# Performance work log

Measured on AMD Instinct MI355X. Metric: run time of the kernel, lower is better.

The kernel has to match this reference:

```python
import jax, jax.numpy as jnp
import numpy as np

N = 50000      # nodes
E = 800000     # edges (before self loops)
NF = 4         # node feature dim
EF = 4         # edge feature dim
EMB = 16       # joint embedding dim
HID = 64       # hidden dim
OUT = 128      # output dim
H = 4          # heads (layers 0,1); last layer has 1 head
NEG_SLOPE = 0.2


def setup_inputs() -> dict:
    key = jax.random.key(0)
    ks = jax.random.split(key, 20)
    in0 = NF + EMB  # 20

    def lin(k, o, i):
        return (jax.random.normal(k, (o, i), jnp.float32) * np.float32(1.0 / np.sqrt(i)))

    return {
        'x': jax.random.normal(ks[0], (N, NF), jnp.float32),
        'edge_index': jax.random.randint(ks[1], (2, E), 0, N, dtype=jnp.int32),
        'edge_attr': jax.random.normal(ks[2], (E, EF), jnp.float32),
        'joint_types': jax.random.randint(ks[3], (N,), 0, 17, dtype=jnp.int32),
        'emb_table': jax.random.normal(ks[4], (17, EMB), jnp.float32) * 0.1,
        'W0': lin(ks[5], H * HID, in0),
        'a_src0': jax.random.normal(ks[6], (H, HID), jnp.float32) * 0.1,
        'a_dst0': jax.random.normal(ks[7], (H, HID), jnp.float32) * 0.1,
        'We0': lin(ks[8], H, EF),
        'W1': lin(ks[9], H * HID, HID),
        'a_src1': jax.random.normal(ks[10], (H, HID), jnp.float32) * 0.1,
        'a_dst1': jax.random.normal(ks[11], (H, HID), jnp.float32) * 0.1,
        'We1': lin(ks[12], H, EF),
        'W2': lin(ks[13], 1 * OUT, HID),
        'a_src2': jax.random.normal(ks[14], (1, OUT), jnp.float32) * 0.1,
        'a_dst2': jax.random.normal(ks[15], (1, OUT), jnp.float32) * 0.1,
        'We2': lin(ks[16], 1, EF),
    }


def gat_layer(x, src, dst, eattr, W, a_src, a_dst, We, num_nodes):
    # x: [N, F_in]; W: [H*C, F_in]; a_src/a_dst: [H, C]; We: [H, EF]
    Hh, C = a_src.shape
    h = (x @ W.T).reshape(num_nodes, Hh, C)  # [N, H, C]
    # per-node attention scores, gathered per edge (same math as per-edge dot)
    s_i = jnp.einsum('nhc,hc->nh', h, a_src)  # applied to x_i = x[dst]
    s_j = jnp.einsum('nhc,hc->nh', h, a_dst)  # applied to x_j = x[src]
    alpha = s_i[dst] + s_j[src] + eattr @ We.T  # [Etot, H]
    alpha = jax.nn.leaky_relu(alpha, NEG_SLOPE)
    # faithful to torch.softmax(alpha, dim=0): GLOBAL softmax over all edges per head
    alpha = jax.nn.softmax(alpha, axis=0)
    msgs = h[src] * alpha[:, :, None]  # [Etot, H, C]
    out = jax.ops.segment_sum(msgs, dst, num_segments=num_nodes)  # aggr='add'
    return out.mean(axis=1)  # update(): mean over heads -> [N, C]


def reference(x, edge_index, edge_attr, joint_types, emb_table,
              W0, a_src0, a_dst0, We0,
              W1, a_src1, a_dst1, We1,
              W2, a_src2, a_dst2, We2):
    num_nodes = x.shape[0]
    # add self loops (edge_attr fill 0.0)
    loops = jnp.arange(num_nodes, dtype=edge_index.dtype)
    src = jnp.concatenate([edge_index[0], loops])
    dst = jnp.concatenate([edge_index[1], loops])
    eattr = jnp.concatenate([edge_attr, jnp.zeros((num_nodes, edge_attr.shape[1]), edge_attr.dtype)], axis=0)

    h = jnp.concatenate([x, emb_table[joint_types]], axis=-1)  # [N, 20]
    h = gat_layer(h, src, dst, eattr, W0, a_src0, a_dst0, We0, num_nodes)
    h = jax.nn.elu(h)  # dropout is identity in eval mode
    h = gat_layer(h, src, dst, eattr, W1, a_src1, a_dst1, We1, num_nodes)
    h = jax.nn.elu(h)
    h = gat_layer(h, src, dst, eattr, W2, a_src2, a_dst2, We2, num_nodes)
    return h  # [N, OUT]
```

## Files before the change

### kernel.cpp

```cpp
#include <hip/hip_runtime.h>
#include <math.h>

#define NN 50000
#define EE 800000
#define EEN (EE+NN)
#define STRIDE 64
#define NFEAT 4
#define EFEAT 4
#define EMBD 16
#define IN0 20
#define HIDD 64
#define OUTD 128

__device__ __forceinline__ unsigned short f2bf(float f){
  unsigned u = __float_as_uint(f);
  return (unsigned short)((u + 0x7FFFu + ((u>>16)&1u)) >> 16);
}
__device__ __forceinline__ float bfl(unsigned u){ return __uint_as_float(u<<16); }
__device__ __forceinline__ float bfh(unsigned u){ return __uint_as_float(u & 0xFFFF0000u); }

template<int V> struct ldt;
template<> struct ldt<4>{ using T = uint2; };
template<> struct ldt<2>{ using T = unsigned int; };

__global__ void k_init(int* fill){
  int i = blockIdx.x*blockDim.x + threadIdx.x;
  if (i < NN) fill[i]=0;
}

__global__ void k_scatter(const int* __restrict__ ei, int* fill,
                          int* __restrict__ col, int* __restrict__ epos){
  int idx = blockIdx.x*blockDim.x + threadIdx.x;
  if (idx < EE){
    int d = ei[EE+idx];
    int pos = atomicAdd(&fill[d],1);
    col[d*STRIDE + 1 + pos] = ei[idx];
    epos[idx] = d*STRIDE + 1 + pos;
  } else if (idx < EEN){
    int n = idx-EE;
    col[n*STRIDE] = n;
  }
}

template<int F_IN,int HH,int CC>
__device__ __forceinline__ void av_one(const float* W, const float* asrc,
                                       const float* adst, float* av, int tid){
  if (tid >= HH*F_IN) return;
  int h = tid / F_IN, f = tid % F_IN;
  float s1=0.f, s2=0.f;
  for (int c=0;c<CC;c++){
    float wv = W[(size_t)(h*CC+c)*F_IN+f];
    s1 += asrc[h*CC+c]*wv;
    s2 += adst[h*CC+c]*wv;
  }
  av[tid] = s1;
  av[HH*F_IN+tid] = s2;
}
__global__ void k_av3(const float* W0, const float* as0, const float* ad0, float* av0,
                      const float* W1, const float* as1, const float* ad1, float* av1,
                      const float* W2, const float* as2, const float* ad2, float* av2,
                      float* zred){
  int tid = threadIdx.x;
  if      (blockIdx.x==0){ av_one<IN0,4,64> (W0, as0, ad0, av0, tid); if (tid<24) zred[tid]=0.f; }
  else if (blockIdx.x==1) av_one<64,4,64>  (W1, as1, ad1, av1, tid);
  else                    av_one<64,1,128> (W2, as2, ad2, av2, tid);
}

template<int K,int NCOL,int HH,bool CONCAT>
__global__ __launch_bounds__(256)
void k_gemm(const float* __restrict__ xin, const int* __restrict__ jt,
            const float* __restrict__ emb, const float* __restrict__ W,
            const float* __restrict__ avp, unsigned short* __restrict__ hout,
            float* __restrict__ si, float* __restrict__ sj){
  constexpr int PITCH = 132;
  __shared__ float xT[K*PITCH];
  __shared__ float wT[K*PITCH];
  __shared__ float EMBL[CONCAT ? 17*EMBD : 1];
  int tid = threadIdx.x;
  int rbase = blockIdx.x*128, cbase = blockIdx.y*128;
  if (CONCAT){
    for (int i=tid; i<17*EMBD; i+=256) EMBL[i]=emb[i];
    __syncthreads();
    if (tid < 128){
      int row = tid;
      int gr = rbase+row; if (gr >= NN) gr = NN-1;
      float4 v = ((const float4*)xin)[gr];
      xT[0*PITCH+row]=v.x; xT[1*PITCH+row]=v.y;
      xT[2*PITCH+row]=v.z; xT[3*PITCH+row]=v.w;
      int j = jt[gr];
      #pragma unroll
      for (int k=0;k<EMBD;k++) xT[(NFEAT+k)*PITCH+row] = EMBL[j*EMBD+k];
    } else {
      int col = tid-128;
      const float4* wp = (const float4*)(W + (size_t)(cbase+col)*K);
      #pragma unroll
      for (int k4=0;k4<K/4;k4++){
        float4 v = wp[k4];
        wT[(4*k4+0)*PITCH+col]=v.x; wT[(4*k4+1)*PITCH+col]=v.y;
        wT[(4*k4+2)*PITCH+col]=v.z; wT[(4*k4+3)*PITCH+col]=v.w;
      }
    }
  } else {
    constexpr int K4 = K/4;
    for (int i=tid; i<128*K4; i+=256){
      int row = i/K4, k4 = i%K4;
      int gr = rbase+row; if (gr >= NN) gr = NN-1;
      float4 v = ((const float4*)xin)[(size_t)gr*K4 + k4];
      xT[(4*k4+0)*PITCH+row]=v.x; xT[(4*k4+1)*PITCH+row]=v.y;
      xT[(4*k4+2)*PITCH+row]=v.z; xT[(4*k4+3)*PITCH+row]=v.w;
    }
    for (int i=tid; i<128*K4; i+=256){
      int col = i/K4, k4 = i%K4;
      float4 v = ((const float4*)W)[(size_t)(cbase+col)*K4 + k4];
      wT[(4*k4+0)*PITCH+col]=v.x; wT[(4*k4+1)*PITCH+col]=v.y;
      wT[(4*k4+2)*PITCH+col]=v.z; wT[(4*k4+3)*PITCH+col]=v.w;
    }
  }
  __syncthreads();
  int lane = tid & 63, w = tid >> 6;
  int r0 = (w>>1)*64 + (lane&7)*8;
  int c0 = (w&1)*64 + (lane>>3)*8;
  float acc[8][8];
  #pragma unroll
  for (int i=0;i<8;i++)
    #pragma unroll
    for (int j=0;j<8;j++) acc[i][j]=0.f;
  #pragma unroll 4
  for (int k=0;k<K;k++){
    float a[8], b[8];
    *(float4*)&a[0] = *(const float4*)&xT[k*PITCH + r0];
    *(float4*)&a[4] = *(const float4*)&xT[k*PITCH + r0 + 4];
    *(float4*)&b[0] = *(const float4*)&wT[k*PITCH + c0];
    *(float4*)&b[4] = *(const float4*)&wT[k*PITCH + c0 + 4];
    #pragma unroll
    for (int i=0;i<8;i++)
      #pragma unroll
      for (int j=0;j<8;j++) acc[i][j] += a[i]*b[j];
  }
  if (blockIdx.y==0 && tid < 128){
    int row = tid, gr = rbase+row;
    if (gr < NN){
      #pragma unroll
      for (int h=0;h<HH;h++){
        float a=0.f, b=0.f;
        for (int k=0;k<K;k++){
          float xv = xT[k*PITCH+row];
          a += xv*avp[h*K+k];
          b += xv*avp[HH*K+h*K+k];
        }
        si[(size_t)gr*HH+h]=a;
        sj[(size_t)gr*HH+h]=b;
      }
    }
  }
  #pragma unroll
  for (int i=0;i<8;i++){
    int n = rbase + r0 + i;
    if (n < NN){
      uint4 o;
      o.x = (unsigned)f2bf(acc[i][0]) | ((unsigned)f2bf(acc[i][1])<<16);
      o.y = (unsigned)f2bf(acc[i][2]) | ((unsigned)f2bf(acc[i][3])<<16);
      o.z = (unsigned)f2bf(acc[i][4]) | ((unsigned)f2bf(acc[i][5])<<16);
      o.w = (unsigned)f2bf(acc[i][6]) | ((unsigned)f2bf(acc[i][7])<<16);
      *(uint4*)(hout + (size_t)n*NCOL + cbase + c0) = o;
    }
  }
}

template<int HH>
__global__ void k_edge(const int* __restrict__ ei, const float* __restrict__ eattr,
                       const float* __restrict__ We, const float* __restrict__ si,
                       const float* __restrict__ sj, const int* __restrict__ epos,
                       float* __restrict__ pp, float* __restrict__ zred){
  int idx = blockIdx.x*blockDim.x + threadIdx.x;
  float z[HH];
  #pragma unroll
  for (int h=0;h<HH;h++) z[h]=0.f;
  if (idx < EE){
    int s = ei[idx], d = ei[EE+idx];
    const float4 ea = ((const float4*)eattr)[idx];
    int pos = epos[idx];
    if (HH==4){
      float4 siv = ((const float4*)si)[d];
      float4 sjv = ((const float4*)sj)[s];
      float te[4] = {siv.x+sjv.x, siv.y+sjv.y, siv.z+sjv.z, siv.w+sjv.w};
      float pv[4];
      #pragma unroll
      for (int h=0;h<4;h++){
        float t = te[h] + ea.x*We[h*EFEAT+0] + ea.y*We[h*EFEAT+1]
                        + ea.z*We[h*EFEAT+2] + ea.w*We[h*EFEAT+3];
        t = (t>0.f)? t : 0.2f*t;
        float p = expf(t);
        z[h]=p; pv[h]=p;
      }
      ((float4*)pp)[pos] = make_float4(pv[0],pv[1],pv[2],pv[3]);
    } else {
      float t = si[d] + sj[s]
              + ea.x*We[0] + ea.y*We[1] + ea.z*We[2] + ea.w*We[3];
      t = (t>0.f)? t : 0.2f*t;
      float p = expf(t);
      z[0]=p;
      pp[pos] = p;
    }
  } else if (idx < EEN){
    int n = idx-EE;
    int pos = n*STRIDE;
    if (HH==4){
      float4 siv = ((const float4*)si)[n];
      float4 sjv = ((const float4*)sj)[n];
      float te[4] = {siv.x+sjv.x, siv.y+sjv.y, siv.z+sjv.z, siv.w+sjv.w};
      float pv[4];
      #pragma unroll
      for (int h=0;h<4;h++){
        float t = te[h];
        t = (t>0.f)? t : 0.2f*t;
        float p = expf(t);
        z[h]=p; pv[h]=p;
      }
      ((float4*)pp)[pos] = make_float4(pv[0],pv[1],pv[2],pv[3]);
    } else {
      float t = si[n]+sj[n];
      t = (t>0.f)? t : 0.2f*t;
      float p = expf(t);
      z[0]=p;
      pp[pos]=p;
    }
  }
  __shared__ float zs[4][HH];
  #pragma unroll
  for (int h=0;h<HH;h++){
    float v=z[h];
    #pragma unroll
    for (int off=32; off>0; off>>=1) v += __shfl_xor(v,off,64);
    if ((threadIdx.x&63)==0) zs[threadIdx.x>>6][h]=v;
  }
  __syncthreads();
  if (threadIdx.x < HH){
    float tot = zs[0][threadIdx.x]+zs[1][threadIdx.x]
              + zs[2][threadIdx.x]+zs[3][threadIdx.x];
    atomicAdd(&zred[threadIdx.x], tot);
  }
}

template<int HH,int CC,bool DO_ELU>
__global__ __launch_bounds__(256)
void k_agg(const unsigned short* __restrict__ hb, const float* __restrict__ pp,
           const float* __restrict__ zred, const int* __restrict__ fill,
           const int* __restrict__ col, float* __restrict__ outp){
  constexpr int HC = HH*CC;
  constexpr int V  = HC/64;
  using LT = typename ldt<V>::T;
  int wave = threadIdx.x>>6, lane = threadIdx.x&63;
  int n = blockIdx.x*4 + wave;
  int hd = (lane*V)/CC;
  float invZ = 1.0f/zred[hd];
  float acc[V];
  #pragma unroll
  for (int v=0;v<V;v++) acc[v]=0.f;
  auto mac = [&](float p, LT h){
    if constexpr (V==4){
      acc[0] += p*bfl(h.x); acc[1] += p*bfh(h.x);
      acc[2] += p*bfl(h.y); acc[3] += p*bfh(h.y);
    } else {
      acc[0] += p*bfl(h);   acc[1] += p*bfh(h);
    }
  };
  int beg = n*STRIDE, end = beg + 1 + fill[n];
  int i = beg;
  for (; i+8<=end; i+=8){
    int sr[8]; float p[8]; LT h[8];
    #pragma unroll
    for (int k=0;k<8;k++) sr[k]=col[i+k];
    #pragma unroll
    for (int k=0;k<8;k++)
      p[k] = (HH==4) ? pp[(size_t)(i+k)*4+hd] : pp[i+k];
    #pragma unroll
    for (int k=0;k<8;k++) h[k]=((const LT*)(hb + (size_t)sr[k]*HC))[lane];
    #pragma unroll
    for (int k=0;k<8;k++) mac(p[k], h[k]);
  }
  for (; i<end; i++){
    int sr = col[i];
    float p = (HH==4) ? pp[(size_t)i*4+hd] : pp[i];
    LT h = ((const LT*)(hb + (size_t)sr*HC))[lane];
    mac(p, h);
  }
  #pragma unroll
  for (int v=0;v<V;v++) acc[v] *= invZ;
  if (HH==4){
    #pragma unroll
    for (int off=16; off<64; off<<=1){
      #pragma unroll
      for (int v=0;v<V;v++) acc[v] += __shfl_xor(acc[v], off, 64);
    }
    if (lane < 16){
      float4 o;
      o.x=0.25f*acc[0]; o.y=0.25f*acc[1]; o.z=0.25f*acc[2]; o.w=0.25f*acc[3];
      if (DO_ELU){
        o.x = (o.x>0.f)? o.x : expm1f(o.x);
        o.y = (o.y>0.f)? o.y : expm1f(o.y);
        o.z = (o.z>0.f)? o.z : expm1f(o.z);
        o.w = (o.w>0.f)? o.w : expm1f(o.w);
      }
      ((float4*)outp)[(size_t)n*(CC/4)+lane] = o;
    }
  } else {
    float2 o; o.x=acc[0]; o.y=acc[1];
    if (DO_ELU){
      o.x = (o.x>0.f)? o.x : expm1f(o.x);
      o.y = (o.y>0.f)? o.y : expm1f(o.y);
    }
    ((float2*)outp)[(size_t)n*(CC/2)+lane] = o;
  }
}

extern "C" void kernel_launch(void* const* d_in, const int* in_sizes, int n_in,
                              void* d_out, int out_size, void* d_ws, size_t ws_size,
                              hipStream_t stream){
  const float* x    = (const float*)d_in[0];
  const int*   ei   = (const int*)d_in[1];
  const float* eatt = (const float*)d_in[2];
  const int*   jt   = (const int*)d_in[3];
  const float* emb  = (const float*)d_in[4];
  const float* W0   = (const float*)d_in[5];
  const float* as0  = (const float*)d_in[6];
  const float* ad0  = (const float*)d_in[7];
  const float* We0  = (const float*)d_in[8];
  const float* W1   = (const float*)d_in[9];
  const float* as1  = (const float*)d_in[10];
  const float* ad1  = (const float*)d_in[11];
  const float* We1  = (const float*)d_in[12];
  const float* W2   = (const float*)d_in[13];
  const float* as2  = (const float*)d_in[14];
  const float* ad2  = (const float*)d_in[15];
  const float* We2  = (const float*)d_in[16];
  float* out = (float*)d_out;

  char* p = (char*)d_ws;
  auto alloc = [&](size_t bytes)->char*{
    char* r = p; p += (bytes + 255) & ~(size_t)255; return r;
  };
  unsigned short* hbuf = (unsigned short*)alloc((size_t)NN*256*2);
  float* x1     = (float*)alloc((size_t)NN*64*4);
  float* x2     = (float*)alloc((size_t)NN*64*4);
  float* si     = (float*)alloc((size_t)NN*4*4);
  float* sj     = (float*)alloc((size_t)NN*4*4);
  float* pp     = (float*)alloc((size_t)NN*STRIDE*16);
  int*   fill   = (int*)alloc((size_t)NN*4);
  int*   col    = (int*)alloc((size_t)NN*STRIDE*4);
  int*   epos   = (int*)alloc((size_t)EE*4);
  float* av0    = (float*)alloc(512*4);
  float* av1    = (float*)alloc(512*4);
  float* av2    = (float*)alloc(512*4);
  float* zred   = (float*)alloc(3*8*4);

  k_init   <<<dim3((NN+255)/256),  256, 0, stream>>>(fill);
  k_scatter<<<dim3((EEN+255)/256), 256, 0, stream>>>(ei, fill, col, epos);
  k_av3    <<<dim3(3),             256, 0, stream>>>(W0,as0,ad0,av0, W1,as1,ad1,av1,
                                                     W2,as2,ad2,av2, zred);

  dim3 gg01((NN+127)/128, 2);
  dim3 gg2 ((NN+127)/128, 1);
  dim3 egrid((EEN+255)/256);
  dim3 agrid(NN/4);

  k_gemm<IN0,256,4,true> <<<gg01, 256, 0, stream>>>(x, jt, emb, W0, av0, hbuf, si, sj);
  k_edge<4>              <<<egrid,256, 0, stream>>>(ei, eatt, We0, si, sj, epos, pp, zred+0);
  k_agg<4,64,true>       <<<agrid,256, 0, stream>>>(hbuf, pp, zred+0, fill, col, x1);

  k_gemm<64,256,4,false> <<<gg01, 256, 0, stream>>>(x1, jt, emb, W1, av1, hbuf, si, sj);
  k_edge<4>              <<<egrid,256, 0, stream>>>(ei, eatt, We1, si, sj, epos, pp, zred+8);
  k_agg<4,64,true>       <<<agrid,256, 0, stream>>>(hbuf, pp, zred+8, fill, col, x2);

  k_gemm<64,128,1,false> <<<gg2,  256, 0, stream>>>(x2, jt, emb, W2, av2, hbuf, si, sj);
  k_edge<1>              <<<egrid,256, 0, stream>>>(ei, eatt, We2, si, sj, epos, pp, zred+16);
  k_agg<1,128,false>     <<<agrid,256, 0, stream>>>(hbuf, pp, zred+16, fill, col, out);
}
```

Baseline: 540.1 us.

## Split each node's edge list across two waves and merge k_init into k_av3

The aggregation kernel now assigns two waves per destination node, each handling half of the node's neighbor list with a 4-wide unroll, and combines the partial sums through shared memory before normalization and output. The goal is more memory-level parallelism and shorter per-wave latency chains on the gather-heavy aggregation. The price is a block-wide barrier, shared-memory traffic, and 512-thread blocks that may cut occupancy or register budget. Separately, zeroing the fill counters is folded into the attention-vector kernel, which removes one launch.

```diff
diff --git a/kernel.cpp b/kernel.cpp
--- a/kernel.cpp
+++ b/kernel.cpp
@@ -22,11 +22,6 @@
 template<int V> struct ldt;
 template<> struct ldt<4>{ using T = uint2; };
 template<> struct ldt<2>{ using T = unsigned int; };
-
-__global__ void k_init(int* fill){
-  int i = blockIdx.x*blockDim.x + threadIdx.x;
-  if (i < NN) fill[i]=0;
-}
 
 __global__ void k_scatter(const int* __restrict__ ei, int* fill,
                           int* __restrict__ col, int* __restrict__ epos){
@@ -59,11 +54,13 @@
 __global__ void k_av3(const float* W0, const float* as0, const float* ad0, float* av0,
                       const float* W1, const float* as1, const float* ad1, float* av1,
                       const float* W2, const float* as2, const float* ad2, float* av2,
-                      float* zred){
+                      int* fill, float* zred){
   int tid = threadIdx.x;
+  int gi = blockIdx.x*256 + tid;
+  if (gi < NN) fill[gi] = 0;
   if      (blockIdx.x==0){ av_one<IN0,4,64> (W0, as0, ad0, av0, tid); if (tid<24) zred[tid]=0.f; }
   else if (blockIdx.x==1) av_one<64,4,64>  (W1, as1, ad1, av1, tid);
-  else                    av_one<64,1,128> (W2, as2, ad2, av2, tid);
+  else if (blockIdx.x==2) av_one<64,1,128> (W2, as2, ad2, av2, tid);
 }
 
 template<int K,int NCOL,int HH,bool CONCAT>
@@ -243,17 +240,19 @@
 }
 
 template<int HH,int CC,bool DO_ELU>
-__global__ __launch_bounds__(256)
+__global__ __launch_bounds__(512)
 void k_agg(const unsigned short* __restrict__ hb, const float* __restrict__ pp,
            const float* __restrict__ zred, const int* __restrict__ fill,
            const int* __restrict__ col, float* __restrict__ outp){
   constexpr int HC = HH*CC;
   constexpr int V  = HC/64;
   using LT = typename ldt<V>::T;
-  int wave = threadIdx.x>>6, lane = threadIdx.x&63;
-  int n = blockIdx.x*4 + wave;
+  __shared__ float sm[8*64*V];
+  int tid = threadIdx.x;
+  int w = tid>>6, lane = tid&63;
+  int n = blockIdx.x*4 + (w>>1);
+  int half = w&1;
   int hd = (lane*V)/CC;
-  float invZ = 1.0f/zred[hd];
   float acc[V];
   #pragma unroll
   for (int v=0;v<V;v++) acc[v]=0.f;
@@ -265,19 +264,22 @@
       acc[0] += p*bfl(h);   acc[1] += p*bfh(h);
     }
   };
-  int beg = n*STRIDE, end = beg + 1 + fill[n];
-  int i = beg;
-  for (; i+8<=end; i+=8){
-    int sr[8]; float p[8]; LT h[8];
-    #pragma unroll
-    for (int k=0;k<8;k++) sr[k]=col[i+k];
-    #pragma unroll
-    for (int k=0;k<8;k++)
+  int beg = n*STRIDE;
+  int cnt = 1 + fill[n];
+  int cA  = (cnt+1)>>1;
+  int i   = beg + (half ? cA : 0);
+  int end = beg + (half ? cnt : cA);
+  for (; i+4<=end; i+=4){
+    int sr[4]; float p[4]; LT h[4];
+    #pragma unroll
+    for (int k=0;k<4;k++) sr[k]=col[i+k];
+    #pragma unroll
+    for (int k=0;k<4;k++)
       p[k] = (HH==4) ? pp[(size_t)(i+k)*4+hd] : pp[i+k];
     #pragma unroll
-    for (int k=0;k<8;k++) h[k]=((const LT*)(hb + (size_t)sr[k]*HC))[lane];
-    #pragma unroll
-    for (int k=0;k<8;k++) mac(p[k], h[k]);
+    for (int k=0;k<4;k++) h[k]=((const LT*)(hb + (size_t)sr[k]*HC))[lane];
+    #pragma unroll
+    for (int k=0;k<4;k++) mac(p[k], h[k]);
   }
   for (; i<end; i++){
     int sr = col[i];
@@ -286,31 +288,39 @@
     mac(p, h);
   }
   #pragma unroll
-  for (int v=0;v<V;v++) acc[v] *= invZ;
-  if (HH==4){
-    #pragma unroll
-    for (int off=16; off<64; off<<=1){
-      #pragma unroll
-      for (int v=0;v<V;v++) acc[v] += __shfl_xor(acc[v], off, 64);
-    }
-    if (lane < 16){
-      float4 o;
-      o.x=0.25f*acc[0]; o.y=0.25f*acc[1]; o.z=0.25f*acc[2]; o.w=0.25f*acc[3];
+  for (int v=0;v<V;v++) sm[(w*64+lane)*V+v] = acc[v];
+  __syncthreads();
+  if (half==0){
+    #pragma unroll
+    for (int v=0;v<V;v++) acc[v] += sm[((w+1)*64+lane)*V+v];
+    float invZ = 1.0f/zred[hd];
+    #pragma unroll
+    for (int v=0;v<V;v++) acc[v] *= invZ;
+    if (HH==4){
+      #pragma unroll
+      for (int off=16; off<64; off<<=1){
+        #pragma unroll
+        for (int v=0;v<V;v++) acc[v] += __shfl_xor(acc[v], off, 64);
+      }
+      if (lane < 16){
+        float4 o;
+        o.x=0.25f*acc[0]; o.y=0.25f*acc[1]; o.z=0.25f*acc[2]; o.w=0.25f*acc[3];
+        if (DO_ELU){
+          o.x = (o.x>0.f)? o.x : expm1f(o.x);
+          o.y = (o.y>0.f)? o.y : expm1f(o.y);
+          o.z = (o.z>0.f)? o.z : expm1f(o.z);
+          o.w = (o.w>0.f)? o.w : expm1f(o.w);
+        }
+        ((float4*)outp)[(size_t)n*(CC/4)+lane] = o;
+      }
+    } else {
+      float2 o; o.x=acc[0]; o.y=acc[1];
       if (DO_ELU){
         o.x = (o.x>0.f)? o.x : expm1f(o.x);
         o.y = (o.y>0.f)? o.y : expm1f(o.y);
-        o.z = (o.z>0.f)? o.z : expm1f(o.z);
-        o.w = (o.w>0.f)? o.w : expm1f(o.w);
-      }
-      ((float4*)outp)[(size_t)n*(CC/4)+lane] = o;
-    }
-  } else {
-    float2 o; o.x=acc[0]; o.y=acc[1];
-    if (DO_ELU){
-      o.x = (o.x>0.f)? o.x : expm1f(o.x);
-      o.y = (o.y>0.f)? o.y : expm1f(o.y);
-    }
-    ((float2*)outp)[(size_t)n*(CC/2)+lane] = o;
+      }
+      ((float2*)outp)[(size_t)n*(CC/2)+lane] = o;
+    }
   }
 }
 
@@ -354,10 +364,9 @@
   float* av2    = (float*)alloc(512*4);
   float* zred   = (float*)alloc(3*8*4);
 
-  k_init   <<<dim3((NN+255)/256),  256, 0, stream>>>(fill);
+  k_av3    <<<dim3((NN+255)/256),  256, 0, stream>>>(W0,as0,ad0,av0, W1,as1,ad1,av1,
+                                                     W2,as2,ad2,av2, fill, zred);
   k_scatter<<<dim3((EEN+255)/256), 256, 0, stream>>>(ei, fill, col, epos);
-  k_av3    <<<dim3(3),             256, 0, stream>>>(W0,as0,ad0,av0, W1,as1,ad1,av1,
-                                                     W2,as2,ad2,av2, zred);
 
   dim3 gg01((NN+127)/128, 2);
   dim3 gg2 ((NN+127)/128, 1);
@@ -366,13 +375,13 @@
 
   k_gemm<IN0,256,4,true> <<<gg01, 256, 0, stream>>>(x, jt, emb, W0, av0, hbuf, si, sj);
   k_edge<4>              <<<egrid,256, 0, stream>>>(ei, eatt, We0, si, sj, epos, pp, zred+0);
-  k_agg<4,64,true>       <<<agrid,256, 0, stream>>>(hbuf, pp, zred+0, fill, col, x1);
+  k_agg<4,64,true>       <<<agrid,512, 0, stream>>>(hbuf, pp, zred+0, fill, col, x1);
 
   k_gemm<64,256,4,false> <<<gg01, 256, 0, stream>>>(x1, jt, emb, W1, av1, hbuf, si, sj);
   k_edge<4>              <<<egrid,256, 0, stream>>>(ei, eatt, We1, si, sj, epos, pp, zred+8);
-  k_agg<4,64,true>       <<<agrid,256, 0, stream>>>(hbuf, pp, zred+8, fill, col, x2);
+  k_agg<4,64,true>       <<<agrid,512, 0, stream>>>(hbuf, pp, zred+8, fill, col, x2);
 
   k_gemm<64,128,1,false> <<<gg2,  256, 0, stream>>>(x2, jt, emb, W2, av2, hbuf, si, sj);
   k_edge<1>              <<<egrid,256, 0, stream>>>(ei, eatt, We2, si, sj, epos, pp, zred+16);
-  k_agg<1,128,false>     <<<agrid,256, 0, stream>>>(hbuf, pp, zred+16, fill, col, out);
-}
+  k_agg<1,128,false>     <<<agrid,512, 0, stream>>>(hbuf, pp, zred+16, fill, col, out);
+}
```

Result: slower. 560.0 us (+3.7%).
